# Kernel tuning notes

Hardware: AMD Instinct MI355X
Metric: run time of the kernel (lower is better)

Reference implementation:

```python
import jax, jax.numpy as jnp
import numpy as np

OUT_H = OUT_W = 14
RATIO = 2
SCALES = (0.25, 0.125, 0.0625, 0.03125)
MIN_LEVEL, MAX_LEVEL = 2, 5
CANON_SIZE, CANON_LEVEL = 224.0, 4.0
IMG = 1024.0


def setup_inputs() -> dict:
    key = jax.random.key(0)
    k0, k1, k2, k3, kc, ks = jax.random.split(key, 6)
    x0 = jax.random.normal(k0, (2, 256, 256, 256), dtype=jnp.float32)
    x1 = jax.random.normal(k1, (2, 256, 128, 128), dtype=jnp.float32)
    x2 = jax.random.normal(k2, (2, 256, 64, 64), dtype=jnp.float32)
    x3 = jax.random.normal(k3, (2, 256, 32, 32), dtype=jnp.float32)
    M = 512
    ctr = jax.random.uniform(kc, (M, 2), minval=0.0, maxval=IMG)
    wh = jax.random.uniform(ks, (M, 2), minval=16.0, maxval=512.0)
    xy0 = jnp.clip(ctr - wh / 2, 0.0, IMG - 1.0)
    xy1 = jnp.clip(ctr + wh / 2, 1.0, IMG)
    bidx = jnp.concatenate([jnp.zeros((M // 2, 1)), jnp.ones((M - M // 2, 1))], axis=0)
    boxes = jnp.concatenate([bidx, xy0[:, :1], xy0[:, 1:], xy1[:, :1], xy1[:, 1:]], axis=1).astype(jnp.float32)
    return {"x0": x0, "x1": x1, "x2": x2, "x3": x3, "boxes": boxes}


def _axis_weights(coords, L):
    # torchvision ROIAlign bilinear edge handling
    valid = (coords >= -1.0) & (coords <= L)
    c = jnp.clip(coords, 0.0, L - 1.0)
    lo = jnp.floor(c)
    hi = jnp.minimum(lo + 1.0, L - 1.0)
    w_hi = c - lo
    w_lo = 1.0 - w_hi
    w_lo = jnp.where(valid, w_lo, 0.0)
    w_hi = jnp.where(valid, w_hi, 0.0)
    return lo.astype(jnp.int32), hi.astype(jnp.int32), w_lo, w_hi


def _roi_align(feat, boxes, scale, ph, pw, ratio, aligned=True):
    # feat: [N,C,H,W], boxes: [M,5] (batch_idx, x0, y0, x1, y1)
    N, C, H, W = feat.shape
    M = boxes.shape[0]
    bidx = boxes[:, 0].astype(jnp.int32)
    off = 0.5 if aligned else 0.0
    x0 = boxes[:, 1] * scale - off
    y0 = boxes[:, 2] * scale - off
    x1 = boxes[:, 3] * scale - off
    y1 = boxes[:, 4] * scale - off
    rw, rh = x1 - x0, y1 - y0
    if not aligned:
        rw = jnp.maximum(rw, 1.0)
        rh = jnp.maximum(rh, 1.0)
    bh, bw = rh / ph, rw / pw
    # fractional bin positions of sample points: [ph*ratio]
    sy = (jnp.arange(ph, dtype=jnp.float32)[:, None]
          + (jnp.arange(ratio, dtype=jnp.float32)[None, :] + 0.5) / ratio).reshape(-1)
    sx = (jnp.arange(pw, dtype=jnp.float32)[:, None]
          + (jnp.arange(ratio, dtype=jnp.float32)[None, :] + 0.5) / ratio).reshape(-1)
    y = y0[:, None] + sy[None, :] * bh[:, None]  # [M, NY]
    x = x0[:, None] + sx[None, :] * bw[:, None]  # [M, NX]
    yl, yh, wyl, wyh = _axis_weights(y, float(H))
    xl, xh, wxl, wxh = _axis_weights(x, float(W))

    def gather(yi, xi):
        # -> [M, NY, NX, C]
        return feat[bidx[:, None, None], :, yi[:, :, None], xi[:, None, :]]

    v = ((wyl[:, :, None] * wxl[:, None, :])[..., None] * gather(yl, xl)
         + (wyl[:, :, None] * wxh[:, None, :])[..., None] * gather(yl, xh)
         + (wyh[:, :, None] * wxl[:, None, :])[..., None] * gather(yh, xl)
         + (wyh[:, :, None] * wxh[:, None, :])[..., None] * gather(yh, xh))
    # average the ratio x ratio samples per output bin
    v = v.reshape(M, ph, ratio, pw, ratio, C).mean(axis=(2, 4))  # [M, ph, pw, C]
    return v.transpose(0, 3, 1, 2)  # [M, C, ph, pw]


def reference(x0, x1, x2, x3, boxes):
    feats = [x0, x1, x2, x3]
    # assign_boxes_to_levels
    bw = boxes[:, 3] - boxes[:, 1]
    bh = boxes[:, 4] - boxes[:, 2]
    sizes = jnp.sqrt(bw * bh)
    lvl = jnp.floor(CANON_LEVEL + jnp.log2(sizes / CANON_SIZE + 1e-8))
    lvl = jnp.clip(lvl, MIN_LEVEL, MAX_LEVEL).astype(jnp.int32) - MIN_LEVEL  # [M]
    out = jnp.zeros((boxes.shape[0], feats[0].shape[1], OUT_H, OUT_W), dtype=x0.dtype)
    for i, (f, s) in enumerate(zip(feats, SCALES)):
        pooled = _roi_align(f, boxes, s, OUT_H, OUT_W, RATIO, aligned=True)
        out = out + jnp.where((lvl == i)[:, None, None, None], pooled, 0.0)
    return out
```

## Files before the change

kernel.cpp:

```cpp
#include <hip/hip_runtime.h>
#include <stdint.h>

#define OUT_HW    14
#define NBINS     196
#define C_TOTAL   256
#define C_PER_BLK 32
#define NQUADS    (C_PER_BLK / 4)
#define NBOXES    512
#define BUFL      1280
#define MAXG      2
#define NSLOT     56

__device__ __forceinline__ void axis_entry(float coord, float L,
                                           int& lo, int& hi, float& wlo, float& whi) {
    const bool valid = (coord >= -1.0f) && (coord <= L);
    const float c   = fminf(fmaxf(coord, 0.0f), L - 1.0f);
    const float flo = floorf(c);
    const float fhi = fminf(flo + 1.0f, L - 1.0f);
    whi = c - flo;
    wlo = 1.0f - whi;
    if (!valid) { wlo = 0.0f; whi = 0.0f; }
    lo = (int)flo;
    hi = (int)fhi;
}

__device__ __forceinline__ unsigned pack_bf16(float a, float b) {
    unsigned ua = __float_as_uint(a);
    unsigned ub = __float_as_uint(b);
    ua += 0x7FFFu + ((ua >> 16) & 1u);
    ub += 0x7FFFu + ((ub >> 16) & 1u);
    return (ua >> 16) | (ub & 0xFFFF0000u);
}
__device__ __forceinline__ float lo16(unsigned u) { return __uint_as_float(u << 16); }
__device__ __forceinline__ float hi16(unsigned u) { return __uint_as_float(u & 0xFFFF0000u); }

__global__ __launch_bounds__(256, 3) void roi_pool_kernel(
    const float* __restrict__ x0, const float* __restrict__ x1,
    const float* __restrict__ x2, const float* __restrict__ x3,
    const float* __restrict__ boxes, float* __restrict__ out)
{
    __shared__ uint2 tile[2][BUFL];

    const int m    = blockIdx.x;
    const int cblk = blockIdx.y;
    const int tid  = threadIdx.x;

    const float bxi = boxes[m*5+0];
    const float bx0 = boxes[m*5+1];
    const float by0 = boxes[m*5+2];
    const float bx1 = boxes[m*5+3];
    const float by1 = boxes[m*5+4];

    const float sz = sqrtf((bx1 - bx0) * (by1 - by0));
    int lvl = (int)floorf(4.0f + log2f(sz * (1.0f/224.0f) + 1e-8f));
    lvl = min(max(lvl, 2), 5) - 2;

    const float scales[4] = {0.25f, 0.125f, 0.0625f, 0.03125f};
    const int   dims[4]   = {256, 128, 64, 32};
    const float scale = scales[lvl];
    const int   W  = dims[lvl];
    const int   HW = W * W;
    const float Lf = (float)W;
    const float* feat = (lvl == 0) ? x0 : (lvl == 1) ? x1 : (lvl == 2) ? x2 : x3;
    const int bidx = (int)bxi;

    const float rx0 = bx0*scale - 0.5f;
    const float ry0 = by0*scale - 0.5f;
    const float binw = (bx1*scale - 0.5f - rx0) * (1.0f/14.0f);
    const float binh = (by1*scale - 0.5f - ry0) * (1.0f/14.0f);

    auto slot_row = [&](int k) {
        const int s = k >> 1;
        const float coord = ry0 + ((float)(s >> 1) + 0.25f + 0.5f*(float)(s & 1)) * binh;
        int lo, hi; float a, b;
        axis_entry(coord, Lf, lo, hi, a, b);
        return (k & 1) ? hi : lo;
    };

    int ymin, ymax, xmin, xmax;
    {
        int lo, hi; float a, b;
        axis_entry(ry0 +  0.25f*binh, Lf, lo, hi, a, b); ymin = lo;
        axis_entry(ry0 + 13.75f*binh, Lf, lo, hi, a, b); ymax = hi;
        axis_entry(rx0 +  0.25f*binw, Lf, lo, hi, a, b); xmin = lo;
        axis_entry(rx0 + 13.75f*binw, Lf, lo, hi, a, b); xmax = hi;
    }
    const int gx  = xmin & ~3;
    const int TW  = (xmax - gx + 1 + 3) & ~3;
    const int TW4 = TW >> 2;
    const int TWL = TW + 1;
    const int NRn = ymax - ymin + 1;
    const bool slotY = (NRn > NSLOT);
    int NRE = slotY ? NSLOT : NRn;
    if (NRE * TWL > BUFL) NRE = BUFL / TWL;
    const int NG  = NRE * TW4;
    const int TCL = NRE * TWL;
    const int CMAX = TCL - 2;

    int  gbase[MAXG];
    int  lbase[MAXG];
    bool gv[MAXG];
    #pragma unroll
    for (int s = 0; s < MAXG; ++s) {
        const int g = tid + (s << 8);
        gv[s] = (g < NG);
        const int gc = min(g, NG - 1);
        const int r  = gc / TW4;
        const int c4 = (gc - r * TW4) << 2;
        const int grow = slotY ? slot_row(r) : (ymin + r);
        gbase[s] = min(grow * W + gx + c4, HW - 4);
        lbase[s] = r * TWL + c4;
    }

    const bool active = (tid < NBINS);
    const int  t  = active ? tid : (NBINS - 1);
    const int  ph = t / OUT_HW;
    const int  pw = t - ph * OUT_HW;

    int yl0, yh0, yl1, yh1, xl0, xh0, xl1, xh1;
    float wy0, wy1, wy2, wy3, wx0, wx1, wx2, wx3;
    axis_entry(ry0 + ((float)ph + 0.25f)*binh, Lf, yl0, yh0, wy0, wy1);
    axis_entry(ry0 + ((float)ph + 0.75f)*binh, Lf, yl1, yh1, wy2, wy3);
    axis_entry(rx0 + ((float)pw + 0.25f)*binw, Lf, xl0, xh0, wx0, wx1);
    axis_entry(rx0 + ((float)pw + 0.75f)*binw, Lf, xl1, xh1, wx2, wx3);
    wy0 *= 0.25f; wy1 *= 0.25f; wy2 *= 0.25f; wy3 *= 0.25f;
    const float wyv[4] = { wy0, wy1, wy2, wy3 };

    int sr[4];
    if (slotY) { sr[0] = 4*ph; sr[1] = 4*ph + 1; sr[2] = 4*ph + 2; sr[3] = 4*ph + 3; }
    else       { sr[0] = yl0 - ymin; sr[1] = yh0 - ymin; sr[2] = yl1 - ymin; sr[3] = yh1 - ymin; }
    const int sc[4] = { xl0 - gx, xh0 - gx, xl1 - gx, xh1 - gx };

    int wq[16];
    #pragma unroll
    for (int i = 0; i < 4; ++i) {
        #pragma unroll
        for (int j = 0; j < 4; ++j) {
            wq[i*4 + j] = min(sr[i] * TWL + sc[j], CMAX);
        }
    }

    const float* fb = feat + ((size_t)bidx * C_TOTAL + (size_t)cblk * C_PER_BLK) * HW;
    float* ob = out + ((size_t)m * C_TOTAL + (size_t)cblk * C_PER_BLK) * NBINS + tid;

    float4 stg[MAXG][4];

    auto LOADQ = [&](int qd) {
        const float* f0 = fb + (size_t)qd * 4 * HW;
        const float* f1 = f0 + HW;
        const float* f2 = f1 + HW;
        const float* f3 = f2 + HW;
        #pragma unroll
        for (int s = 0; s < MAXG; ++s) {
            stg[s][0] = *(const float4*)(f0 + gbase[s]);
            stg[s][1] = *(const float4*)(f1 + gbase[s]);
            stg[s][2] = *(const float4*)(f2 + gbase[s]);
            stg[s][3] = *(const float4*)(f3 + gbase[s]);
        }
    };
    auto WRITEQ = [&](uint2* dst) {
        #pragma unroll
        for (int s = 0; s < MAXG; ++s)
            if (gv[s]) {
                uint2* d = dst + lbase[s];
                d[0] = make_uint2(pack_bf16(stg[s][0].x, stg[s][1].x),
                                  pack_bf16(stg[s][2].x, stg[s][3].x));
                d[1] = make_uint2(pack_bf16(stg[s][0].y, stg[s][1].y),
                                  pack_bf16(stg[s][2].y, stg[s][3].y));
                d[2] = make_uint2(pack_bf16(stg[s][0].z, stg[s][1].z),
                                  pack_bf16(stg[s][2].z, stg[s][3].z));
                d[3] = make_uint2(pack_bf16(stg[s][0].w, stg[s][1].w),
                                  pack_bf16(stg[s][2].w, stg[s][3].w));
            }
    };

    LOADQ(0);
    WRITEQ(&tile[0][0]);

    for (int p = 0; p < NQUADS; ++p) {
        const bool more = (p + 1 < NQUADS);
        if (more) LOADQ(p + 1);

        __syncthreads();

        const uint2* bp = &tile[p & 1][0];
        float vx = 0.0f, vy = 0.0f, vz = 0.0f, vw = 0.0f;
        #pragma unroll
        for (int i = 0; i < 4; ++i) {
            const uint2 c0 = bp[wq[4*i + 0]];
            const uint2 c1 = bp[wq[4*i + 1]];
            const uint2 c2 = bp[wq[4*i + 2]];
            const uint2 c3 = bp[wq[4*i + 3]];
            const float wyi = wyv[i];
            vx += wyi * (wx0*lo16(c0.x) + wx1*lo16(c1.x) + wx2*lo16(c2.x) + wx3*lo16(c3.x));
            vy += wyi * (wx0*hi16(c0.x) + wx1*hi16(c1.x) + wx2*hi16(c2.x) + wx3*hi16(c3.x));
            vz += wyi * (wx0*lo16(c0.y) + wx1*lo16(c1.y) + wx2*lo16(c2.y) + wx3*lo16(c3.y));
            vw += wyi * (wx0*hi16(c0.y) + wx1*hi16(c1.y) + wx2*hi16(c2.y) + wx3*hi16(c3.y));
        }
        if (active) {
            ob[(size_t)(4*p + 0) * NBINS] = vx;
            ob[(size_t)(4*p + 1) * NBINS] = vy;
            ob[(size_t)(4*p + 2) * NBINS] = vz;
            ob[(size_t)(4*p + 3) * NBINS] = vw;
        }
        if (more) WRITEQ(&tile[(p + 1) & 1][0]);
    }
}

extern "C" void kernel_launch(void* const* d_in, const int* in_sizes, int n_in,
                              void* d_out, int out_size, void* d_ws, size_t ws_size,
                              hipStream_t stream) {
    const float* x0    = (const float*)d_in[0];
    const float* x1    = (const float*)d_in[1];
    const float* x2    = (const float*)d_in[2];
    const float* x3    = (const float*)d_in[3];
    const float* boxes = (const float*)d_in[4];
    float* out = (float*)d_out;

    dim3 grid(NBOXES, C_TOTAL / C_PER_BLK);
    dim3 block(256);
    roi_pool_kernel<<<grid, block, 0, stream>>>(x0, x1, x2, x3, boxes, out);
}
```

Measured before the change: 72.86 us.

## Pack eight bf16 channels per shared-memory cell and process channel octets

The shared tile changes from uint2 to uint4 cells, so each cell holds eight bf16 channels instead of four. The main loop now covers channel octets, which halves the number of iterations and barriers, and each bilinear tap becomes one 16-byte LDS read. Next-octet global loads and half-writes are interleaved between the two halves of the compute to overlap memory with arithmetic. In exchange, shared memory per block doubles, which could limit occupancy, and live registers increase.

```diff
diff --git a/kernel.cpp b/kernel.cpp
--- a/kernel.cpp
+++ b/kernel.cpp
@@ -5,7 +5,7 @@
 #define NBINS     196
 #define C_TOTAL   256
 #define C_PER_BLK 32
-#define NQUADS    (C_PER_BLK / 4)
+#define NOCT      (C_PER_BLK / 8)
 #define NBOXES    512
 #define BUFL      1280
 #define MAXG      2
@@ -39,7 +39,7 @@
     const float* __restrict__ x2, const float* __restrict__ x3,
     const float* __restrict__ boxes, float* __restrict__ out)
 {
-    __shared__ uint2 tile[2][BUFL];
+    __shared__ uint4 tile[2][BUFL];
 
     const int m    = blockIdx.x;
     const int cblk = blockIdx.y;
@@ -158,52 +158,90 @@
             stg[s][3] = *(const float4*)(f3 + gbase[s]);
         }
     };
-    auto WRITEQ = [&](uint2* dst) {
+    auto WRITEH = [&](uint4* dst, int half) {
+        uint2* d2 = (uint2*)dst;
         #pragma unroll
         for (int s = 0; s < MAXG; ++s)
             if (gv[s]) {
-                uint2* d = dst + lbase[s];
-                d[0] = make_uint2(pack_bf16(stg[s][0].x, stg[s][1].x),
-                                  pack_bf16(stg[s][2].x, stg[s][3].x));
-                d[1] = make_uint2(pack_bf16(stg[s][0].y, stg[s][1].y),
-                                  pack_bf16(stg[s][2].y, stg[s][3].y));
-                d[2] = make_uint2(pack_bf16(stg[s][0].z, stg[s][1].z),
-                                  pack_bf16(stg[s][2].z, stg[s][3].z));
-                d[3] = make_uint2(pack_bf16(stg[s][0].w, stg[s][1].w),
-                                  pack_bf16(stg[s][2].w, stg[s][3].w));
+                const int b = (lbase[s] << 1) + half;
+                d2[b + 0] = make_uint2(pack_bf16(stg[s][0].x, stg[s][1].x),
+                                       pack_bf16(stg[s][2].x, stg[s][3].x));
+                d2[b + 2] = make_uint2(pack_bf16(stg[s][0].y, stg[s][1].y),
+                                       pack_bf16(stg[s][2].y, stg[s][3].y));
+                d2[b + 4] = make_uint2(pack_bf16(stg[s][0].z, stg[s][1].z),
+                                       pack_bf16(stg[s][2].z, stg[s][3].z));
+                d2[b + 6] = make_uint2(pack_bf16(stg[s][0].w, stg[s][1].w),
+                                       pack_bf16(stg[s][2].w, stg[s][3].w));
             }
     };
 
     LOADQ(0);
-    WRITEQ(&tile[0][0]);
-
-    for (int p = 0; p < NQUADS; ++p) {
-        const bool more = (p + 1 < NQUADS);
-        if (more) LOADQ(p + 1);
+    WRITEH(&tile[0][0], 0);
+    LOADQ(1);
+    WRITEH(&tile[0][0], 1);
+
+    for (int o = 0; o < NOCT; ++o) {
+        const bool more = (o + 1 < NOCT);
+        if (more) LOADQ(2*o + 2);
 
         __syncthreads();
 
-        const uint2* bp = &tile[p & 1][0];
-        float vx = 0.0f, vy = 0.0f, vz = 0.0f, vw = 0.0f;
-        #pragma unroll
-        for (int i = 0; i < 4; ++i) {
-            const uint2 c0 = bp[wq[4*i + 0]];
-            const uint2 c1 = bp[wq[4*i + 1]];
-            const uint2 c2 = bp[wq[4*i + 2]];
-            const uint2 c3 = bp[wq[4*i + 3]];
+        const uint4* bp = &tile[o & 1][0];
+        uint4* bn = &tile[(o + 1) & 1][0];
+        float v0 = 0, v1 = 0, v2 = 0, v3 = 0, v4 = 0, v5 = 0, v6 = 0, v7 = 0;
+
+        #pragma unroll
+        for (int i = 0; i < 2; ++i) {
+            const uint4 c0 = bp[wq[4*i + 0]];
+            const uint4 c1 = bp[wq[4*i + 1]];
+            const uint4 c2 = bp[wq[4*i + 2]];
+            const uint4 c3 = bp[wq[4*i + 3]];
             const float wyi = wyv[i];
-            vx += wyi * (wx0*lo16(c0.x) + wx1*lo16(c1.x) + wx2*lo16(c2.x) + wx3*lo16(c3.x));
-            vy += wyi * (wx0*hi16(c0.x) + wx1*hi16(c1.x) + wx2*hi16(c2.x) + wx3*hi16(c3.x));
-            vz += wyi * (wx0*lo16(c0.y) + wx1*lo16(c1.y) + wx2*lo16(c2.y) + wx3*lo16(c3.y));
-            vw += wyi * (wx0*hi16(c0.y) + wx1*hi16(c1.y) + wx2*hi16(c2.y) + wx3*hi16(c3.y));
-        }
+            v0 += wyi * (wx0*lo16(c0.x) + wx1*lo16(c1.x) + wx2*lo16(c2.x) + wx3*lo16(c3.x));
+            v1 += wyi * (wx0*hi16(c0.x) + wx1*hi16(c1.x) + wx2*hi16(c2.x) + wx3*hi16(c3.x));
+            v2 += wyi * (wx0*lo16(c0.y) + wx1*lo16(c1.y) + wx2*lo16(c2.y) + wx3*lo16(c3.y));
+            v3 += wyi * (wx0*hi16(c0.y) + wx1*hi16(c1.y) + wx2*hi16(c2.y) + wx3*hi16(c3.y));
+            v4 += wyi * (wx0*lo16(c0.z) + wx1*lo16(c1.z) + wx2*lo16(c2.z) + wx3*lo16(c3.z));
+            v5 += wyi * (wx0*hi16(c0.z) + wx1*hi16(c1.z) + wx2*hi16(c2.z) + wx3*hi16(c3.z));
+            v6 += wyi * (wx0*lo16(c0.w) + wx1*lo16(c1.w) + wx2*lo16(c2.w) + wx3*lo16(c3.w));
+            v7 += wyi * (wx0*hi16(c0.w) + wx1*hi16(c1.w) + wx2*hi16(c2.w) + wx3*hi16(c3.w));
+        }
+
+        if (more) {
+            WRITEH(bn, 0);
+            LOADQ(2*o + 3);
+        }
+
+        #pragma unroll
+        for (int i = 2; i < 4; ++i) {
+            const uint4 c0 = bp[wq[4*i + 0]];
+            const uint4 c1 = bp[wq[4*i + 1]];
+            const uint4 c2 = bp[wq[4*i + 2]];
+            const uint4 c3 = bp[wq[4*i + 3]];
+            const float wyi = wyv[i];
+            v0 += wyi * (wx0*lo16(c0.x) + wx1*lo16(c1.x) + wx2*lo16(c2.x) + wx3*lo16(c3.x));
+            v1 += wyi * (wx0*hi16(c0.x) + wx1*hi16(c1.x) + wx2*hi16(c2.x) + wx3*hi16(c3.x));
+            v2 += wyi * (wx0*lo16(c0.y) + wx1*lo16(c1.y) + wx2*lo16(c2.y) + wx3*lo16(c3.y));
+            v3 += wyi * (wx0*hi16(c0.y) + wx1*hi16(c1.y) + wx2*hi16(c2.y) + wx3*hi16(c3.y));
+            v4 += wyi * (wx0*lo16(c0.z) + wx1*lo16(c1.z) + wx2*lo16(c2.z) + wx3*lo16(c3.z));
+            v5 += wyi * (wx0*hi16(c0.z) + wx1*hi16(c1.z) + wx2*hi16(c2.z) + wx3*hi16(c3.z));
+            v6 += wyi * (wx0*lo16(c0.w) + wx1*lo16(c1.w) + wx2*lo16(c2.w) + wx3*lo16(c3.w));
+            v7 += wyi * (wx0*hi16(c0.w) + wx1*hi16(c1.w) + wx2*hi16(c2.w) + wx3*hi16(c3.w));
+        }
+
         if (active) {
-            ob[(size_t)(4*p + 0) * NBINS] = vx;
-            ob[(size_t)(4*p + 1) * NBINS] = vy;
-            ob[(size_t)(4*p + 2) * NBINS] = vz;
-            ob[(size_t)(4*p + 3) * NBINS] = vw;
-        }
-        if (more) WRITEQ(&tile[(p + 1) & 1][0]);
+            float* oc = ob + (size_t)(8*o) * NBINS;
+            oc[0]                  = v0;
+            oc[(size_t)1 * NBINS]  = v1;
+            oc[(size_t)2 * NBINS]  = v2;
+            oc[(size_t)3 * NBINS]  = v3;
+            oc[(size_t)4 * NBINS]  = v4;
+            oc[(size_t)5 * NBINS]  = v5;
+            oc[(size_t)6 * NBINS]  = v6;
+            oc[(size_t)7 * NBINS]  = v7;
+        }
+
+        if (more) WRITEH(bn, 1);
     }
 }
 
```

New measurement: 79.93 us. 1.1x slower.
